# Kernel tuning notes

Hardware: AMD Instinct MI355X
Metric: run time of the kernel (lower is better)

The kernel has to match this reference:

```python
import jax, jax.numpy as jnp
import numpy as np

N_HASHES = 4
CHUNK = 144
REDUCTION = 4
RES_SCALE = 1.0
NORM_EPS = 5e-5


def conv2d(x, w, b, pad):
    y = jax.lax.conv_general_dilated(
        x, w, window_strides=(1, 1), padding=[(pad, pad), (pad, pad)],
        dimension_numbers=('NCHW', 'OIHW', 'NCHW'))
    return y + b[None, :, None, None]


def add_adjacent_buckets(x):
    # x: (N, h, n_chunks, chunk, e); concat each chunk with its circular neighbors
    back = jnp.roll(x, 1, axis=2)
    fwd = jnp.roll(x, -1, axis=2)
    return jnp.concatenate([x, back, fwd], axis=3)


def setup_inputs() -> dict:
    key = jax.random.key(0)
    ks = jax.random.split(key, 6)
    x = jax.random.normal(ks[0], (1, 32, 192, 192), jnp.float32)
    w_match = jax.random.normal(ks[1], (8, 32, 3, 3), jnp.float32) * 0.05
    b_match = jnp.zeros((8,), jnp.float32)
    w_asm = jax.random.normal(ks[2], (32, 32, 1, 1), jnp.float32) * 0.05
    b_asm = jnp.zeros((32,), jnp.float32)
    rotations = jax.random.normal(ks[3], (8, N_HASHES, 64), jnp.float32)
    return {'x': x, 'w_match': w_match, 'b_match': b_match,
            'w_asm': w_asm, 'b_asm': b_asm, 'rotations': rotations}


def reference(x, w_match, b_match, w_asm, b_asm, rotations):
    N, _, H, W = x.shape
    L = H * W
    # conv_match: 3x3 conv 32->8; conv_assembly: 1x1 conv 32->32
    x_embed = conv2d(x, w_match, b_match, 1).reshape(N, -1, L).transpose(0, 2, 1)  # (N, L, 8)
    y_embed = conv2d(x, w_asm, b_asm, 0).reshape(N, -1, L).transpose(0, 2, 1)      # (N, L, 32)
    C = x_embed.shape[-1]
    hash_buckets = min(L // CHUNK + (L // CHUNK) % 2, 128)  # = 128 here

    # --- LSH hashing (non-differentiable; rotations passed in for determinism) ---
    rotated = jnp.einsum('blf,fhi->bhli', x_embed, rotations)        # (N, h, L, hb/2)
    rotated = jnp.concatenate([rotated, -rotated], axis=-1)          # (N, h, L, hb)
    hash_codes = jnp.argmax(rotated, axis=-1)                        # (N, h, L)
    hash_codes = hash_codes + (jnp.arange(N_HASHES) * hash_buckets)[None, :, None]
    hash_codes = hash_codes.reshape(N, -1)                           # (N, h*L)

    # --- sort tokens by bucket id ---
    indices = jnp.argsort(hash_codes, axis=-1)
    undo_sort = jnp.argsort(indices, axis=-1)
    mod_indices = indices % L
    x_sorted = jnp.take_along_axis(x_embed, mod_indices[:, :, None], axis=1)  # (N, h*L, 8)
    y_sorted = jnp.take_along_axis(y_embed, mod_indices[:, :, None], axis=1)  # (N, h*L, 32)

    x_b = x_sorted.reshape(N, N_HASHES, -1, C)
    y_b = y_sorted.reshape(N, N_HASHES, -1, C * REDUCTION)
    padding = (-L) % CHUNK  # static; 0 for L=192*192
    if padding:
        x_b = jnp.concatenate([x_b, x_b[:, :, -padding:, :]], axis=2)
        y_b = jnp.concatenate([y_b, y_b[:, :, -padding:, :]], axis=2)
    x_b = x_b.reshape(N, N_HASHES, -1, CHUNK, C)
    y_b = y_b.reshape(N, N_HASHES, -1, CHUNK, C * REDUCTION)

    # --- bucketed attention with adjacent buckets ---
    nrm = jnp.linalg.norm(x_b, axis=-1, keepdims=True)
    x_match = x_b / jnp.maximum(nrm, NORM_EPS)   # F.normalize(eps=5e-5)
    x_match = add_adjacent_buckets(x_match)      # (N, h, k, 3*chunk, 8)
    y_adj = add_adjacent_buckets(y_b)            # (N, h, k, 3*chunk, 32)

    raw = jnp.einsum('bhkie,bhkje->bhkij', x_b, x_match)  # (N, h, k, 144, 432)
    bucket_score = jax.scipy.special.logsumexp(raw, axis=-1, keepdims=True)
    score = jnp.exp(raw - bucket_score)
    ret = jnp.einsum('bhkij,bhkje->bhkie', score, y_adj)  # (N, h, k, 144, 32)

    ret = ret.reshape(N, N_HASHES, -1, C * REDUCTION)
    bucket_score = bucket_score.reshape(N, N_HASHES, -1)
    if padding:
        ret = ret[:, :, :-padding, :]
        bucket_score = bucket_score[:, :, :-padding]
    ret = ret.reshape(N, -1, C * REDUCTION)
    bucket_score = bucket_score.reshape(N, -1)

    # --- unsort and combine hash rounds via softmax over logsumexp scores ---
    ret = jnp.take_along_axis(ret, undo_sort[:, :, None], axis=1)
    bucket_score = jnp.take_along_axis(bucket_score, undo_sort, axis=1)
    ret = ret.reshape(N, N_HASHES, L, C * REDUCTION)
    probs = jax.nn.softmax(bucket_score.reshape(N, N_HASHES, L, 1), axis=1)
    out = jnp.sum(ret * probs, axis=1)                     # (N, L, 32)
    out = out.transpose(0, 2, 1).reshape(N, -1, H, W) * RES_SCALE + x
    return out
```

## Files before the change

### kernel.cpp

```cpp
#include <hip/hip_runtime.h>
#include <hip/hip_bf16.h>
#include <math.h>

#define LTOT 36864
#define NH 4
#define NCHUNK 256
#define CHU 144
#define NBUCK 128
#define NSEG 144
#define HW_ 192
#define VTS 148

typedef unsigned int u32;
typedef unsigned short u16;
typedef unsigned long long u64;
typedef __attribute__((ext_vector_type(4))) short short4v;
typedef __attribute__((ext_vector_type(4))) float f32x4;

__device__ __forceinline__ u32 pkbf(float a, float b){
  union { __hip_bfloat162 h2; u32 u; } cv;
  cv.h2 = __float22bfloat162_rn(float2{a,b});
  return cv.u;
}
__device__ __forceinline__ float bflo(u32 w){ return __uint_as_float(w<<16); }
__device__ __forceinline__ float bfhi(u32 w){ return __uint_as_float(w & 0xffff0000u); }

__global__ __launch_bounds__(512) void k_conv(const float* __restrict__ x,
    const float* __restrict__ wm, const float* __restrict__ bm,
    const float* __restrict__ wa, const float* __restrict__ ba,
    const float* __restrict__ rot,
    float* __restrict__ xe, u16* __restrict__ Vu, int* __restrict__ code,
    int* __restrict__ hist)
{
  __shared__ float xs[32*108];
  __shared__ float xq[64*8];
  const int t = threadIdx.x;
  const int id = blockIdx.x;
  const int bx = id % 12, by = id / 12;

  for (int idx=t; idx<3456; idx+=512){
    int ci = idx/108, rem = idx-ci*108;
    int iy = rem/18,  ix = rem-iy*18;
    int yy = by*4+iy-1, xx = bx*16+ix-1;
    float v = 0.f;
    if (yy>=0 && yy<HW_ && xx>=0 && xx<HW_) v = x[ci*LTOT + yy*HW_ + xx];
    xs[idx] = v;
  }
  __syncthreads();
  const int lane = t & 63;
  const int w  = __builtin_amdgcn_readfirstlane(t>>6);
  const int co = w;
  const int cb = 4*w;
  const int ix = lane & 15, iy = lane >> 4;
  float a0 = bm[co];
  float acc[4];
  #pragma unroll
  for (int j=0;j<4;j++) acc[j] = ba[cb+j];
  const float* xb  = xs + iy*18 + ix;
  const float* w0p = wm + co*288;
  for (int ci=0; ci<32; ci++){
    const float* xp = xb + ci*108;
    float x00=xp[0],  x01=xp[1],  x02=xp[2];
    float x10=xp[18], x11=xp[19], x12=xp[20];
    float x20=xp[36], x21=xp[37], x22=xp[38];
    const float* w0 = w0p + ci*9;
    a0 += x00*w0[0]+x01*w0[1]+x02*w0[2]
        + x10*w0[3]+x11*w0[4]+x12*w0[5]
        + x20*w0[6]+x21*w0[7]+x22*w0[8];
    const float* wap = wa + cb*32 + ci;
    #pragma unroll
    for (int j=0;j<4;j++) acc[j] += x11 * wap[j*32];
  }
  const int l = (by*4+iy)*HW_ + bx*16+ix;
  xe[l*8 + co] = a0;
  xq[lane*8 + co] = a0;
  uint2 vv;
  vv.x = pkbf(acc[0],acc[1]); vv.y = pkbf(acc[2],acc[3]);
  *(uint2*)(Vu + (size_t)l*32 + cb) = vv;
  __syncthreads();

  if (t < 256){
    const int h = w;
    const float4* qp = (const float4*)(xq + lane*8);
    float4 qa = qp[0], qb = qp[1];
    float best = -INFINITY; int bi = 0;
    float worst = INFINITY; int wi = 0;
    for (int i=0; i<64; i++){
      const float* rp = rot + h*64 + i;
      float v = qa.x*rp[0]    + qa.y*rp[256]  + qa.z*rp[512]  + qa.w*rp[768]
              + qb.x*rp[1024] + qb.y*rp[1280] + qb.z*rp[1536] + qb.w*rp[1792];
      if (v > best)  { best  = v; bi = i; }
      if (v < worst) { worst = v; wi = i; }
    }
    int c = (-worst > best) ? (64+wi) : bi;
    const int ly = lane >> 4, lx = lane & 15;
    const int lpix = (by*4+ly)*HW_ + bx*16+lx;
    code[h*LTOT + lpix] = c;
    atomicAdd(&hist[(h*NSEG + (lpix>>8))*NBUCK + c], 1);
  }
}

__global__ __launch_bounds__(256) void k_scatter(const int* __restrict__ code,
    const int* __restrict__ hist,
    const float* __restrict__ xe, const u16* __restrict__ Vu,
    int* __restrict__ spos, u16* __restrict__ Ks, u16* __restrict__ Qs,
    u16* __restrict__ Vs)
{
  const int h = blockIdx.y, seg = blockIdx.x, t = threadIdx.x;
  const int l = seg*256 + t;
  int c = code[h*LTOT + l];

  __shared__ int pre2[2][NBUCK], tot2[2][NBUCK];
  __shared__ int scv[NBUCK];
  __shared__ int segbase[NBUCK];
  __shared__ int wh[4][NBUCK];

  {
    const int b = t & 127, gg = t >> 7;
    int pre = 0, tt = 0;
    const int sA = gg*72;
    for (int s = sA; s < sA+72; s++){
      int v = hist[(h*NSEG+s)*NBUCK + b];
      tt += v;
      if (s < seg) pre += v;
    }
    pre2[gg][b] = pre; tot2[gg][b] = tt;
  }
  const int lane = t & 63, w = t >> 6;
  u64 mask = ~0ull;
  #pragma unroll
  for (int bit=0; bit<7; bit++){
    u64 bset = __ballot((c>>bit)&1);
    mask &= ((c>>bit)&1) ? bset : ~bset;
  }
  int rin = __popcll(mask & ((lane==0)?0ull:(~0ull >> (64-lane))));
  int cnt = __popcll(mask);
  ((int*)wh)[t] = 0; ((int*)wh)[t+256] = 0;
  __syncthreads();

  if (rin == 0) wh[w][c] = cnt;
  if (t < NBUCK){
    int tt = tot2[0][t] + tot2[1][t];
    int v = tt;
    #pragma unroll
    for (int off=1; off<64; off<<=1){
      int u = __shfl_up(v, off);
      if ((t & 63) >= off) v += u;
    }
    scv[t] = v;
  }
  __syncthreads();

  if (t < NBUCK){
    int tt = tot2[0][t] + tot2[1][t];
    int excl = scv[t] - tt + ((t >= 64) ? scv[63] : 0);
    segbase[t] = excl + pre2[0][t] + pre2[1][t];
  }
  __syncthreads();

  int r = segbase[c] + rin;
  for (int ww=0; ww<w; ww++) r += wh[ww][c];
  spos[h*LTOT + r] = l;

  const float4* xr = (const float4*)(xe + l*8);
  float4 a = xr[0], b = xr[1];
  float n2 = a.x*a.x+a.y*a.y+a.z*a.z+a.w*a.w
           + b.x*b.x+b.y*b.y+b.z*b.z+b.w*b.w;
  float sc = 1.0f / fmaxf(sqrtf(n2), 5e-5f);
  uint4 kk, qq;
  kk.x = pkbf(a.x*sc,a.y*sc); kk.y = pkbf(a.z*sc,a.w*sc);
  kk.z = pkbf(b.x*sc,b.y*sc); kk.w = pkbf(b.z*sc,b.w*sc);
  qq.x = pkbf(a.x,a.y); qq.y = pkbf(a.z,a.w);
  qq.z = pkbf(b.x,b.y); qq.w = pkbf(b.z,b.w);
  *(uint4*)(Ks + (size_t)(h*LTOT + r)*8) = kk;
  *(uint4*)(Qs + (size_t)(h*LTOT + r)*8) = qq;

  const uint4* vr = (const uint4*)(Vu + (size_t)l*32);
  uint4* vp = (uint4*)(Vs + (size_t)(h*LTOT + r)*32);
  vp[0] = vr[0]; vp[1] = vr[1]; vp[2] = vr[2]; vp[3] = vr[3];
}

__global__ __launch_bounds__(320) void k_attn(const u16* __restrict__ Ks,
    const u16* __restrict__ Qs, const u16* __restrict__ Vs,
    const int* __restrict__ spos, u16* __restrict__ ret_u, float* __restrict__ bs_u)
{
  __shared__ __align__(16) u16 Klds[432*8];
  __shared__ __align__(16) u16 Qlds[CHU*8];
  __shared__ __align__(16) u16 VT[3][32*VTS];
  __shared__ float qn[CHU];
  __shared__ int spos_l[CHU];

  const int t = threadIdx.x;
  const int k = blockIdx.x, h = blockIdx.y;

  if (t < CHU){
    uint4 qv = *(const uint4*)(Qs + (size_t)(h*LTOT + k*CHU + t)*8);
    *(uint4*)(Qlds + t*8) = qv;
    float f0=bflo(qv.x), f1=bfhi(qv.x), f2=bflo(qv.y), f3=bfhi(qv.y);
    float f4=bflo(qv.z), f5=bfhi(qv.z), f6=bflo(qv.w), f7=bfhi(qv.w);
    qn[t] = sqrtf(f0*f0+f1*f1+f2*f2+f3*f3+f4*f4+f5*f5+f6*f6+f7*f7)*1.01f + 1e-6f;
    spos_l[t] = spos[h*LTOT + k*CHU + t];
    #pragma unroll
    for (int rr=0; rr<3; rr++){
      const int gkb = ((k + NCHUNK-1 + rr) & (NCHUNK-1)) * CHU;
      *(uint4*)(Klds + (rr*CHU + t)*8) =
          *(const uint4*)(Ks + (size_t)(h*LTOT + gkb + t)*8);
    }
  }
  for (int j = t; j < 432; j += 320){
    int p = j >> 1, hf = j & 1;
    int g = 2*p;
    int rg = g / CHU, lk = g - rg*CHU;
    const int gkb = ((k + NCHUNK-1 + rg) & (NCHUNK-1)) * CHU;
    const uint4* ra = (const uint4*)(Vs + (size_t)(h*LTOT + gkb + lk)*32);
    const uint4* rb = (const uint4*)(Vs + (size_t)(h*LTOT + gkb + lk+1)*32);
    uint4 A0 = ra[hf*2], A1 = ra[hf*2+1];
    uint4 B0 = rb[hf*2], B1 = rb[hf*2+1];
    u32 aw[8] = {A0.x,A0.y,A0.z,A0.w,A1.x,A1.y,A1.z,A1.w};
    u32 bw[8] = {B0.x,B0.y,B0.z,B0.w,B1.x,B1.y,B1.z,B1.w};
    int ebase = hf*16;
    u16* vtb = (u16*)VT[rg];
    #pragma unroll
    for (int m=0;m<8;m++){
      u32 al = aw[m]&0xffffu, ah = aw[m]>>16;
      u32 bl = bw[m]&0xffffu, bh = bw[m]>>16;
      *(u32*)&vtb[(ebase+2*m  )*VTS + lk] = al | (bl<<16);
      *(u32*)&vtb[(ebase+2*m+1)*VTS + lk] = ah | (bh<<16);
    }
  }
  __syncthreads();

  const int lane = t & 63;
  const int wv = t >> 6;
  const int q = lane & 15;
  const int quad = lane >> 4;
  const bool two = (wv < 4);
  const int tl0 = 2*wv;
  const int tl1 = two ? (2*wv+1) : 8;

  const short4v zs = {0,0,0,0};
  short4v bq0 = zs, bq1 = zs;
  if (quad < 2){
    bq0 = *(const short4v*)(Qlds + (tl0*16+q)*8 + quad*4);
    if (two) bq1 = *(const short4v*)(Qlds + (tl1*16+q)*8 + quad*4);
  }
  const float m0 = qn[tl0*16+q];
  const float m1 = two ? qn[tl1*16+q] : 0.f;

  f32x4 o00={0,0,0,0}, o01={0,0,0,0}, o10={0,0,0,0}, o11={0,0,0,0};
  float s0 = 0.f, s1 = 0.f;

  #pragma unroll 3
  for (int kt=0; kt<27; kt++){
    const int rg = kt / 9, ktl = kt - rg*9;
    const u16* vtb = VT[rg];
    short4v av = zs;
    if (quad < 2) av = *(const short4v*)(Klds + (kt*16+q)*8 + quad*4);
    f32x4 zc = {0.f,0.f,0.f,0.f};
    f32x4 stA = __builtin_amdgcn_mfma_f32_16x16x16bf16_1k(av, bq0, zc, 0,0,0);

    float pA0 = __expf(stA[0]-m0), pA1 = __expf(stA[1]-m0);
    float pA2 = __expf(stA[2]-m0), pA3 = __expf(stA[3]-m0);
    s0 += (pA0+pA1)+(pA2+pA3);
    union { u32 u[2]; short4v s4; } pkA;
    pkA.u[0] = pkbf(pA0,pA1); pkA.u[1] = pkbf(pA2,pA3);

    short4v va0 = *(const short4v*)(&vtb[ q    *VTS + ktl*16 + quad*4]);
    short4v va1 = *(const short4v*)(&vtb[(q+16)*VTS + ktl*16 + quad*4]);
    o00 = __builtin_amdgcn_mfma_f32_16x16x16bf16_1k(va0, pkA.s4, o00, 0,0,0);
    o01 = __builtin_amdgcn_mfma_f32_16x16x16bf16_1k(va1, pkA.s4, o01, 0,0,0);

    if (two){
      f32x4 stB = __builtin_amdgcn_mfma_f32_16x16x16bf16_1k(av, bq1, zc, 0,0,0);
      float pB0 = __expf(stB[0]-m1), pB1 = __expf(stB[1]-m1);
      float pB2 = __expf(stB[2]-m1), pB3 = __expf(stB[3]-m1);
      s1 += (pB0+pB1)+(pB2+pB3);
      union { u32 u[2]; short4v s4; } pkB;
      pkB.u[0] = pkbf(pB0,pB1); pkB.u[1] = pkbf(pB2,pB3);
      o10 = __builtin_amdgcn_mfma_f32_16x16x16bf16_1k(va0, pkB.s4, o10, 0,0,0);
      o11 = __builtin_amdgcn_mfma_f32_16x16x16bf16_1k(va1, pkB.s4, o11, 0,0,0);
    }
  }

  float st0 = s0;
  st0 += __shfl_xor(st0, 16); st0 += __shfl_xor(st0, 32);
  float inv0 = 1.0f/st0;

  const int pos0 = spos_l[tl0*16 + q];
  u16* rp0 = ret_u + (size_t)(h*LTOT + pos0)*32;
  uint2 wA, wB;
  wA.x = pkbf(o00[0]*inv0, o00[1]*inv0); wA.y = pkbf(o00[2]*inv0, o00[3]*inv0);
  wB.x = pkbf(o01[0]*inv0, o01[1]*inv0); wB.y = pkbf(o01[2]*inv0, o01[3]*inv0);
  *(uint2*)&rp0[quad*4]    = wA;
  *(uint2*)&rp0[16+quad*4] = wB;
  if (quad == 0) bs_u[h*LTOT + pos0] = m0 + __logf(st0);

  if (two){
    float st1 = s1;
    st1 += __shfl_xor(st1, 16); st1 += __shfl_xor(st1, 32);
    float inv1 = 1.0f/st1;
    const int pos1 = spos_l[tl1*16 + q];
    u16* rp1 = ret_u + (size_t)(h*LTOT + pos1)*32;
    wA.x = pkbf(o10[0]*inv1, o10[1]*inv1); wA.y = pkbf(o10[2]*inv1, o10[3]*inv1);
    wB.x = pkbf(o11[0]*inv1, o11[1]*inv1); wB.y = pkbf(o11[2]*inv1, o11[3]*inv1);
    *(uint2*)&rp1[quad*4]    = wA;
    *(uint2*)&rp1[16+quad*4] = wB;
    if (quad == 0) bs_u[h*LTOT + pos1] = m1 + __logf(st1);
  }
}

__global__ __launch_bounds__(256) void k_final(const float* __restrict__ x,
    const u16* __restrict__ ret_u, const float* __restrict__ bs_u,
    float* __restrict__ out)
{
  const int l  = blockIdx.x*64 + (threadIdx.x & 63);
  const int eg = threadIdx.x >> 6;
  float bs[NH];
  #pragma unroll
  for (int h=0;h<NH;h++) bs[h] = bs_u[h*LTOT + l];
  float m = fmaxf(fmaxf(bs[0],bs[1]), fmaxf(bs[2],bs[3]));
  float p[NH]; float s = 0.f;
  #pragma unroll
  for (int h=0;h<NH;h++){ p[h] = __expf(bs[h]-m); s += p[h]; }
  float inv = 1.0f/s;
  float o[8];
  #pragma unroll
  for (int e=0;e<8;e++) o[e]=0.f;
  #pragma unroll
  for (int h=0;h<NH;h++){
    float w = p[h]*inv;
    uint4 v = *(const uint4*)(ret_u + (size_t)(h*LTOT + l)*32 + eg*8);
    o[0] += w*bflo(v.x); o[1] += w*bfhi(v.x);
    o[2] += w*bflo(v.y); o[3] += w*bfhi(v.y);
    o[4] += w*bflo(v.z); o[5] += w*bfhi(v.z);
    o[6] += w*bflo(v.w); o[7] += w*bfhi(v.w);
  }
  #pragma unroll
  for (int e=0;e<8;e++){
    int ge = eg*8 + e;
    out[ge*LTOT + l] = o[e] + x[ge*LTOT + l];
  }
}

extern "C" void kernel_launch(void* const* d_in, const int* in_sizes, int n_in,
                              void* d_out, int out_size, void* d_ws, size_t ws_size,
                              hipStream_t stream)
{
  const float* x   = (const float*)d_in[0];
  const float* wm  = (const float*)d_in[1];
  const float* bm  = (const float*)d_in[2];
  const float* wa  = (const float*)d_in[3];
  const float* ba  = (const float*)d_in[4];
  const float* rot = (const float*)d_in[5];
  float* out = (float*)d_out;

  char* ws = (char*)d_ws;
  size_t off = 0;
  auto alloc = [&](size_t bytes)->void*{
    void* p = ws + off;
    off = (off + bytes + 255) & ~(size_t)255;
    return p;
  };
  float* xe     = (float*)alloc((size_t)LTOT*8*4);
  u16*   Vu     = (u16*)  alloc((size_t)LTOT*32*2);
  int*   code   = (int*)  alloc((size_t)NH*LTOT*4);
  int*   hist   = (int*)  alloc((size_t)NH*NSEG*NBUCK*4);
  int*   spos   = (int*)  alloc((size_t)NH*LTOT*4);
  u16*   Ks     = (u16*)  alloc((size_t)NH*LTOT*8*2);
  u16*   Qs     = (u16*)  alloc((size_t)NH*LTOT*8*2);
  u16*   Vs     = (u16*)  alloc((size_t)NH*LTOT*32*2);
  u16*   ret_u  = (u16*)  alloc((size_t)NH*LTOT*32*2);
  float* bs_u   = (float*)alloc((size_t)NH*LTOT*4);

  hipMemsetAsync(hist, 0, (size_t)NH*NSEG*NBUCK*4, stream);
  hipLaunchKernelGGL(k_conv,    dim3(576),        dim3(512), 0, stream, x, wm, bm, wa, ba, rot, xe, Vu, code, hist);
  hipLaunchKernelGGL(k_scatter, dim3(NSEG,NH),    dim3(256), 0, stream, code, hist, xe, Vu, spos, Ks, Qs, Vs);
  hipLaunchKernelGGL(k_attn,    dim3(NCHUNK,NH),  dim3(320), 0, stream, Ks, Qs, Vs, spos, ret_u, bs_u);
  hipLaunchKernelGGL(k_final,   dim3(576),        dim3(256), 0, stream, x, ret_u, bs_u, out);
}
```

Baseline: 134.4 us.

## Gather K/Q/V via sorted indices in attention instead of materializing sorted copies

The scatter kernel no longer writes sorted per-hash copies of K, Q and V. It now only computes sorted positions (spos). The conv kernel computes normalized K and bf16 Q once per pixel. The attention kernel gathers these rows indirectly through spos. The conv kernel is also reshaped to 256 threads, with each wave computing two match channels and eight assembly channels. This removes a large write-then-read of 4x-replicated sorted buffers, at the cost of uncoalesced random gathers in the attention load phase.

```diff
diff --git a/kernel.cpp b/kernel.cpp
--- a/kernel.cpp
+++ b/kernel.cpp
@@ -25,12 +25,12 @@
 __device__ __forceinline__ float bflo(u32 w){ return __uint_as_float(w<<16); }
 __device__ __forceinline__ float bfhi(u32 w){ return __uint_as_float(w & 0xffff0000u); }
 
-__global__ __launch_bounds__(512) void k_conv(const float* __restrict__ x,
+__global__ __launch_bounds__(256) void k_conv(const float* __restrict__ x,
     const float* __restrict__ wm, const float* __restrict__ bm,
     const float* __restrict__ wa, const float* __restrict__ ba,
     const float* __restrict__ rot,
-    float* __restrict__ xe, u16* __restrict__ Vu, int* __restrict__ code,
-    int* __restrict__ hist)
+    u16* __restrict__ Ku, u16* __restrict__ Qu, u16* __restrict__ Vu,
+    int* __restrict__ code, int* __restrict__ hist)
 {
   __shared__ float xs[32*108];
   __shared__ float xq[64*8];
@@ -38,7 +38,7 @@
   const int id = blockIdx.x;
   const int bx = id % 12, by = id / 12;
 
-  for (int idx=t; idx<3456; idx+=512){
+  for (int idx=t; idx<3456; idx+=256){
     int ci = idx/108, rem = idx-ci*108;
     int iy = rem/18,  ix = rem-iy*18;
     int yy = by*4+iy-1, xx = bx*16+ix-1;
@@ -49,37 +49,58 @@
   __syncthreads();
   const int lane = t & 63;
   const int w  = __builtin_amdgcn_readfirstlane(t>>6);
-  const int co = w;
-  const int cb = 4*w;
+  const int co0 = 2*w, cb = 8*w;
   const int ix = lane & 15, iy = lane >> 4;
-  float a0 = bm[co];
-  float acc[4];
-  #pragma unroll
-  for (int j=0;j<4;j++) acc[j] = ba[cb+j];
+  float a0 = bm[co0], a1 = bm[co0+1];
+  float acc[8];
+  #pragma unroll
+  for (int co=0;co<8;co++) acc[co] = ba[cb+co];
   const float* xb  = xs + iy*18 + ix;
-  const float* w0p = wm + co*288;
+  const float* w0p = wm + co0*288;
+  const float* w1p = w0p + 288;
   for (int ci=0; ci<32; ci++){
     const float* xp = xb + ci*108;
     float x00=xp[0],  x01=xp[1],  x02=xp[2];
     float x10=xp[18], x11=xp[19], x12=xp[20];
     float x20=xp[36], x21=xp[37], x22=xp[38];
     const float* w0 = w0p + ci*9;
+    const float* w1 = w1p + ci*9;
     a0 += x00*w0[0]+x01*w0[1]+x02*w0[2]
         + x10*w0[3]+x11*w0[4]+x12*w0[5]
         + x20*w0[6]+x21*w0[7]+x22*w0[8];
+    a1 += x00*w1[0]+x01*w1[1]+x02*w1[2]
+        + x10*w1[3]+x11*w1[4]+x12*w1[5]
+        + x20*w1[6]+x21*w1[7]+x22*w1[8];
     const float* wap = wa + cb*32 + ci;
     #pragma unroll
-    for (int j=0;j<4;j++) acc[j] += x11 * wap[j*32];
+    for (int co=0;co<8;co++) acc[co] += x11 * wap[co*32];
   }
   const int l = (by*4+iy)*HW_ + bx*16+ix;
-  xe[l*8 + co] = a0;
-  xq[lane*8 + co] = a0;
-  uint2 vv;
+  *(float2*)(xq + lane*8 + co0) = float2{a0,a1};
+  uint4 vv;
   vv.x = pkbf(acc[0],acc[1]); vv.y = pkbf(acc[2],acc[3]);
-  *(uint2*)(Vu + (size_t)l*32 + cb) = vv;
-  __syncthreads();
-
-  if (t < 256){
+  vv.z = pkbf(acc[4],acc[5]); vv.w = pkbf(acc[6],acc[7]);
+  *(uint4*)(Vu + (size_t)l*32 + cb) = vv;
+  __syncthreads();
+
+  if (t < 64){
+    const int ly = t >> 4, lx = t & 15;
+    const int lp = (by*4+ly)*HW_ + bx*16+lx;
+    const float4* qp = (const float4*)(xq + t*8);
+    float4 a = qp[0], b = qp[1];
+    float n2 = a.x*a.x+a.y*a.y+a.z*a.z+a.w*a.w
+             + b.x*b.x+b.y*b.y+b.z*b.z+b.w*b.w;
+    float sc = 1.0f / fmaxf(sqrtf(n2), 5e-5f);
+    uint4 kk, qq;
+    kk.x = pkbf(a.x*sc,a.y*sc); kk.y = pkbf(a.z*sc,a.w*sc);
+    kk.z = pkbf(b.x*sc,b.y*sc); kk.w = pkbf(b.z*sc,b.w*sc);
+    qq.x = pkbf(a.x,a.y); qq.y = pkbf(a.z,a.w);
+    qq.z = pkbf(b.x,b.y); qq.w = pkbf(b.z,b.w);
+    *(uint4*)(Ku + (size_t)lp*8) = kk;
+    *(uint4*)(Qu + (size_t)lp*8) = qq;
+  }
+
+  {
     const int h = w;
     const float4* qp = (const float4*)(xq + lane*8);
     float4 qa = qp[0], qb = qp[1];
@@ -100,11 +121,8 @@
   }
 }
 
-__global__ __launch_bounds__(256) void k_scatter(const int* __restrict__ code,
-    const int* __restrict__ hist,
-    const float* __restrict__ xe, const u16* __restrict__ Vu,
-    int* __restrict__ spos, u16* __restrict__ Ks, u16* __restrict__ Qs,
-    u16* __restrict__ Vs)
+__global__ __launch_bounds__(256) void k_spos(const int* __restrict__ code,
+    const int* __restrict__ hist, int* __restrict__ spos)
 {
   const int h = blockIdx.y, seg = blockIdx.x, t = threadIdx.x;
   const int l = seg*256 + t;
@@ -161,27 +179,10 @@
   int r = segbase[c] + rin;
   for (int ww=0; ww<w; ww++) r += wh[ww][c];
   spos[h*LTOT + r] = l;
-
-  const float4* xr = (const float4*)(xe + l*8);
-  float4 a = xr[0], b = xr[1];
-  float n2 = a.x*a.x+a.y*a.y+a.z*a.z+a.w*a.w
-           + b.x*b.x+b.y*b.y+b.z*b.z+b.w*b.w;
-  float sc = 1.0f / fmaxf(sqrtf(n2), 5e-5f);
-  uint4 kk, qq;
-  kk.x = pkbf(a.x*sc,a.y*sc); kk.y = pkbf(a.z*sc,a.w*sc);
-  kk.z = pkbf(b.x*sc,b.y*sc); kk.w = pkbf(b.z*sc,b.w*sc);
-  qq.x = pkbf(a.x,a.y); qq.y = pkbf(a.z,a.w);
-  qq.z = pkbf(b.x,b.y); qq.w = pkbf(b.z,b.w);
-  *(uint4*)(Ks + (size_t)(h*LTOT + r)*8) = kk;
-  *(uint4*)(Qs + (size_t)(h*LTOT + r)*8) = qq;
-
-  const uint4* vr = (const uint4*)(Vu + (size_t)l*32);
-  uint4* vp = (uint4*)(Vs + (size_t)(h*LTOT + r)*32);
-  vp[0] = vr[0]; vp[1] = vr[1]; vp[2] = vr[2]; vp[3] = vr[3];
-}
-
-__global__ __launch_bounds__(320) void k_attn(const u16* __restrict__ Ks,
-    const u16* __restrict__ Qs, const u16* __restrict__ Vs,
+}
+
+__global__ __launch_bounds__(320) void k_attn(const u16* __restrict__ Ku,
+    const u16* __restrict__ Qu, const u16* __restrict__ Vu,
     const int* __restrict__ spos, u16* __restrict__ ret_u, float* __restrict__ bs_u)
 {
   __shared__ __align__(16) u16 Klds[432*8];
@@ -194,17 +195,18 @@
   const int k = blockIdx.x, h = blockIdx.y;
 
   if (t < CHU){
-    uint4 qv = *(const uint4*)(Qs + (size_t)(h*LTOT + k*CHU + t)*8);
+    int pos0 = spos[h*LTOT + k*CHU + t];
+    spos_l[t] = pos0;
+    uint4 qv = *(const uint4*)(Qu + (size_t)pos0*8);
     *(uint4*)(Qlds + t*8) = qv;
     float f0=bflo(qv.x), f1=bfhi(qv.x), f2=bflo(qv.y), f3=bfhi(qv.y);
     float f4=bflo(qv.z), f5=bfhi(qv.z), f6=bflo(qv.w), f7=bfhi(qv.w);
     qn[t] = sqrtf(f0*f0+f1*f1+f2*f2+f3*f3+f4*f4+f5*f5+f6*f6+f7*f7)*1.01f + 1e-6f;
-    spos_l[t] = spos[h*LTOT + k*CHU + t];
     #pragma unroll
     for (int rr=0; rr<3; rr++){
       const int gkb = ((k + NCHUNK-1 + rr) & (NCHUNK-1)) * CHU;
-      *(uint4*)(Klds + (rr*CHU + t)*8) =
-          *(const uint4*)(Ks + (size_t)(h*LTOT + gkb + t)*8);
+      int pk = spos[h*LTOT + gkb + t];
+      *(uint4*)(Klds + (rr*CHU + t)*8) = *(const uint4*)(Ku + (size_t)pk*8);
     }
   }
   for (int j = t; j < 432; j += 320){
@@ -212,8 +214,10 @@
     int g = 2*p;
     int rg = g / CHU, lk = g - rg*CHU;
     const int gkb = ((k + NCHUNK-1 + rg) & (NCHUNK-1)) * CHU;
-    const uint4* ra = (const uint4*)(Vs + (size_t)(h*LTOT + gkb + lk)*32);
-    const uint4* rb = (const uint4*)(Vs + (size_t)(h*LTOT + gkb + lk+1)*32);
+    int posA = spos[h*LTOT + gkb + lk];
+    int posB = spos[h*LTOT + gkb + lk + 1];
+    const uint4* ra = (const uint4*)(Vu + (size_t)posA*32);
+    const uint4* rb = (const uint4*)(Vu + (size_t)posB*32);
     uint4 A0 = ra[hf*2], A1 = ra[hf*2+1];
     uint4 B0 = rb[hf*2], B1 = rb[hf*2+1];
     u32 aw[8] = {A0.x,A0.y,A0.z,A0.w,A1.x,A1.y,A1.z,A1.w};
@@ -361,20 +365,18 @@
     off = (off + bytes + 255) & ~(size_t)255;
     return p;
   };
-  float* xe     = (float*)alloc((size_t)LTOT*8*4);
+  u16*   Ku     = (u16*)  alloc((size_t)LTOT*8*2);
+  u16*   Qu     = (u16*)  alloc((size_t)LTOT*8*2);
   u16*   Vu     = (u16*)  alloc((size_t)LTOT*32*2);
   int*   code   = (int*)  alloc((size_t)NH*LTOT*4);
   int*   hist   = (int*)  alloc((size_t)NH*NSEG*NBUCK*4);
   int*   spos   = (int*)  alloc((size_t)NH*LTOT*4);
-  u16*   Ks     = (u16*)  alloc((size_t)NH*LTOT*8*2);
-  u16*   Qs     = (u16*)  alloc((size_t)NH*LTOT*8*2);
-  u16*   Vs     = (u16*)  alloc((size_t)NH*LTOT*32*2);
   u16*   ret_u  = (u16*)  alloc((size_t)NH*LTOT*32*2);
   float* bs_u   = (float*)alloc((size_t)NH*LTOT*4);
 
   hipMemsetAsync(hist, 0, (size_t)NH*NSEG*NBUCK*4, stream);
-  hipLaunchKernelGGL(k_conv,    dim3(576),        dim3(512), 0, stream, x, wm, bm, wa, ba, rot, xe, Vu, code, hist);
-  hipLaunchKernelGGL(k_scatter, dim3(NSEG,NH),    dim3(256), 0, stream, code, hist, xe, Vu, spos, Ks, Qs, Vs);
-  hipLaunchKernelGGL(k_attn,    dim3(NCHUNK,NH),  dim3(320), 0, stream, Ks, Qs, Vs, spos, ret_u, bs_u);
-  hipLaunchKernelGGL(k_final,   dim3(576),        dim3(256), 0, stream, x, ret_u, bs_u, out);
-}
+  hipLaunchKernelGGL(k_conv,   dim3(576),        dim3(256), 0, stream, x, wm, bm, wa, ba, rot, Ku, Qu, Vu, code, hist);
+  hipLaunchKernelGGL(k_spos,   dim3(NSEG,NH),    dim3(256), 0, stream, code, hist, spos);
+  hipLaunchKernelGGL(k_attn,   dim3(NCHUNK,NH),  dim3(320), 0, stream, Ku, Qu, Vu, spos, ret_u, bs_u);
+  hipLaunchKernelGGL(k_final,  dim3(576),        dim3(256), 0, stream, x, ret_u, bs_u, out);
+}
```

Measured after the change: 125.8 us. 1.07x faster.
